# Performance work log

Hardware: AMD Instinct MI355X
Metric: run time of the kernel (lower is better)

## Reference

```python
import jax, jax.numpy as jnp
import numpy as np

B = 262144   # n_batch
DT = 0.01    # filter period T_filter from reset_state


def _quat_mul(q, r):
    # Hamilton product, q,r: [B,4] in (w,x,y,z)
    w1, x1, y1, z1 = q[:, 0], q[:, 1], q[:, 2], q[:, 3]
    w2, x2, y2, z2 = r[:, 0], r[:, 1], r[:, 2], r[:, 3]
    return jnp.stack([
        w1 * w2 - x1 * x2 - y1 * y2 - z1 * z2,
        w1 * x2 + x1 * w2 + y1 * z2 - z1 * y2,
        w1 * y2 - x1 * z2 + y1 * w2 + z1 * x2,
        w1 * z2 + x1 * y2 - y1 * x2 + z1 * w2,
    ], axis=-1)


def _inject(state, err):
    # state: [B,7,1] = [p(3); q(4)], err: [B,6,1] = [dp(3); dtheta(3)]
    p = state[:, :3, 0] + err[:, :3, 0]
    q = state[:, 3:, 0]
    dth = 0.5 * err[:, 3:, 0]
    dq = jnp.concatenate([jnp.ones_like(dth[:, :1]), dth], axis=-1)  # small-angle quat
    qn = _quat_mul(q, dq)
    qn = qn / jnp.linalg.norm(qn, axis=-1, keepdims=True)
    return jnp.concatenate([p, qn], axis=-1)[:, :, None]


def _Xdx(state):
    # ESKF Jacobian of nominal state wrt error state: [B,7,6]
    q = state[:, 3:, 0]
    bsz = q.shape[0]
    w, xq, y, z = q[:, 0], q[:, 1], q[:, 2], q[:, 3]
    Qd = 0.5 * jnp.stack([
        jnp.stack([-xq, -y, -z], -1),
        jnp.stack([w, -z, y], -1),
        jnp.stack([z, w, -xq], -1),
        jnp.stack([-y, xq, w], -1),
    ], axis=1)  # [B,4,3]
    I3 = jnp.broadcast_to(jnp.eye(3, dtype=state.dtype), (bsz, 3, 3))
    top = jnp.concatenate([I3, jnp.zeros((bsz, 3, 3), state.dtype)], axis=-1)
    bot = jnp.concatenate([jnp.zeros((bsz, 4, 3), state.dtype), Qd], axis=-1)
    return jnp.concatenate([top, bot], axis=1)


def setup_inputs() -> dict:
    key = jax.random.key(0)
    k1, k2, k3 = jax.random.split(key, 3)
    x = jax.random.normal(k1, (14, B), dtype=jnp.float32)
    p = jax.random.normal(k2, (B, 3), dtype=jnp.float32)
    q = jax.random.normal(k3, (B, 4), dtype=jnp.float32)
    q = q / jnp.linalg.norm(q, axis=-1, keepdims=True)
    state = jnp.concatenate([p, q], axis=-1)[:, :, None]  # [B,7,1]
    # covariances as in reset_state (diagonal, batched)
    covariance = jnp.tile(jnp.diag(jnp.array([1e-3] * 3 + [0.2] * 3, jnp.float32))[None], (B, 1, 1))
    Q = jnp.tile(jnp.diag(jnp.array([1e-4] * 3 + [2e-4] * 3, jnp.float32))[None], (B, 1, 1))
    R = jnp.tile(jnp.diag(jnp.array([1e-6] * 3 + [1e-4] * 4, jnp.float32))[None], (B, 1, 1))
    return {"x": x, "state": state, "covariance": covariance, "Q": Q, "R": R}


def reference(x, state, covariance, Q, R):
    # --- unpack forward args (mirrors forward(): permute(2,1,0)) ---
    twist = x[8:14].T[:, :, None]        # [B,6,1] control
    measurement = x[0:7].T[:, :, None]   # [B,7,1]
    # --- predict: F = I6, B_matrix = dt * I6 ---
    error_state_prior = DT * twist                       # B_matrix @ u
    predict_state = _inject(state, error_state_prior)    # [B,7,1]
    P = covariance + Q                                   # F P F^T + Q with F = I
    # --- update ---
    H = _Xdx(state)                                      # Hx = I7, so H = Xdx: [B,7,6]
    Ht = jnp.swapaxes(H, 1, 2)                           # [B,6,7]
    S = H @ P @ Ht + R                                   # [B,7,7]
    K = P @ Ht @ jnp.linalg.inv(S)                       # [B,6,7]
    innovation = measurement - predict_state             # [B,7,1]
    error_state = K @ innovation                         # [B,6,1]
    I6 = jnp.eye(6, dtype=P.dtype)
    P_new = (I6[None] - K @ H) @ P                       # stored as self.covariance (side effect)
    new_state = _inject(predict_state, error_state)      # [B,7,1]
    del P_new  # forward() returns only the state
    return new_state
```

## Files before the change

### kernel.cpp

```cpp
#include <hip/hip_runtime.h>

#define DT_C 0.01f

__global__ __launch_bounds__(256) void eskf_kernel(
    const float* __restrict__ x,
    const float* __restrict__ state,
    const float* __restrict__ cov,
    const float* __restrict__ Qm,
    const float* __restrict__ Rm,
    float* __restrict__ out,
    int B)
{
    int b = blockIdx.x * blockDim.x + threadIdx.x;
    if (b >= B) return;

    float meas[7];
#pragma unroll
    for (int i = 0; i < 7; ++i) meas[i] = x[i * B + b];
    float tw[6];
#pragma unroll
    for (int i = 0; i < 6; ++i) tw[i] = x[(8 + i) * B + b];
    float st[7];
#pragma unroll
    for (int i = 0; i < 7; ++i) st[i] = state[b * 7 + i];

    float P[36];
    {
        const float4* c4 = (const float4*)(cov + (size_t)b * 36);
        const float4* q4 = (const float4*)(Qm  + (size_t)b * 36);
#pragma unroll
        for (int i = 0; i < 9; ++i) {
            float4 a = c4[i], bb = q4[i];
            P[4*i+0] = a.x + bb.x;
            P[4*i+1] = a.y + bb.y;
            P[4*i+2] = a.z + bb.z;
            P[4*i+3] = a.w + bb.w;
        }
    }

    float S[7][7];
    {
        const float* r = Rm + (size_t)b * 49;
#pragma unroll
        for (int i = 0; i < 7; ++i)
#pragma unroll
            for (int j = 0; j < 7; ++j)
                S[i][j] = r[i * 7 + j];
    }

    float ps[7];
    {
        float d0 = 0.5f * DT_C * tw[3], d1 = 0.5f * DT_C * tw[4], d2 = 0.5f * DT_C * tw[5];
        ps[0] = st[0] + DT_C * tw[0];
        ps[1] = st[1] + DT_C * tw[1];
        ps[2] = st[2] + DT_C * tw[2];
        float w = st[3], xx = st[4], yy = st[5], zz = st[6];
        float qw = w - xx * d0 - yy * d1 - zz * d2;
        float qx = w * d0 + xx + yy * d2 - zz * d1;
        float qy = w * d1 - xx * d2 + yy + zz * d0;
        float qz = w * d2 + xx * d1 - yy * d0 + zz;
        float inv = rsqrtf(qw * qw + qx * qx + qy * qy + qz * qz);
        ps[3] = qw * inv; ps[4] = qx * inv; ps[5] = qy * inv; ps[6] = qz * inv;
    }

    float Qd[4][3];
    {
        float w = st[3], xx = st[4], yy = st[5], zz = st[6];
        Qd[0][0] = -0.5f * xx; Qd[0][1] = -0.5f * yy; Qd[0][2] = -0.5f * zz;
        Qd[1][0] =  0.5f * w;  Qd[1][1] = -0.5f * zz; Qd[1][2] =  0.5f * yy;
        Qd[2][0] =  0.5f * zz; Qd[2][1] =  0.5f * w;  Qd[2][2] = -0.5f * xx;
        Qd[3][0] = -0.5f * yy; Qd[3][1] =  0.5f * xx; Qd[3][2] =  0.5f * w;
    }

#pragma unroll
    for (int i = 0; i < 3; ++i)
#pragma unroll
        for (int j = 0; j < 3; ++j)
            S[i][j] += P[i * 6 + j];

    float T[4][6];
#pragma unroll
    for (int i = 0; i < 4; ++i)
#pragma unroll
        for (int c = 0; c < 6; ++c) {
            float acc = 0.f;
#pragma unroll
            for (int k = 0; k < 3; ++k) acc += Qd[i][k] * P[(3 + k) * 6 + c];
            T[i][c] = acc;
        }

#pragma unroll
    for (int i = 0; i < 4; ++i)
#pragma unroll
        for (int j = 0; j < 3; ++j) S[3 + i][j] += T[i][j];

#pragma unroll
    for (int i = 0; i < 3; ++i)
#pragma unroll
        for (int j = 0; j < 4; ++j) {
            float acc = 0.f;
#pragma unroll
            for (int k = 0; k < 3; ++k) acc += P[i * 6 + 3 + k] * Qd[j][k];
            S[i][3 + j] += acc;
        }

#pragma unroll
    for (int i = 0; i < 4; ++i)
#pragma unroll
        for (int j = 0; j < 4; ++j) {
            float acc = 0.f;
#pragma unroll
            for (int l = 0; l < 3; ++l) acc += T[i][3 + l] * Qd[j][l];
            S[3 + i][3 + j] += acc;
        }

    float y[7];
#pragma unroll
    for (int i = 0; i < 7; ++i) y[i] = meas[i] - ps[i];

#pragma unroll
    for (int k = 0; k < 7; ++k) {
        float inv = 1.0f / S[k][k];
#pragma unroll
        for (int i = k + 1; i < 7; ++i) {
            float f = S[i][k] * inv;
#pragma unroll
            for (int j = k + 1; j < 7; ++j) S[i][j] -= f * S[k][j];
            y[i] -= f * y[k];
        }
    }
#pragma unroll
    for (int k = 6; k >= 0; --k) {
        float acc = y[k];
#pragma unroll
        for (int j = k + 1; j < 7; ++j) acc -= S[k][j] * y[j];
        y[k] = acc / S[k][k];
    }

    float z6[6];
    z6[0] = y[0]; z6[1] = y[1]; z6[2] = y[2];
#pragma unroll
    for (int c = 0; c < 3; ++c) {
        float acc = 0.f;
#pragma unroll
        for (int i = 0; i < 4; ++i) acc += Qd[i][c] * y[3 + i];
        z6[3 + c] = acc;
    }
    float es[6];
#pragma unroll
    for (int i = 0; i < 6; ++i) {
        float acc = 0.f;
#pragma unroll
        for (int j = 0; j < 6; ++j) acc += P[i * 6 + j] * z6[j];
        es[i] = acc;
    }

    float o0 = ps[0] + es[0];
    float o1 = ps[1] + es[1];
    float o2 = ps[2] + es[2];
    float d0 = 0.5f * es[3], d1 = 0.5f * es[4], d2 = 0.5f * es[5];
    float w = ps[3], xx = ps[4], yy = ps[5], zz = ps[6];
    float qw = w - xx * d0 - yy * d1 - zz * d2;
    float qx = w * d0 + xx + yy * d2 - zz * d1;
    float qy = w * d1 - xx * d2 + yy + zz * d0;
    float qz = w * d2 + xx * d1 - yy * d0 + zz;
    float inv = rsqrtf(qw * qw + qx * qx + qy * qy + qz * qz);

    float* o = out + (size_t)b * 7;
    o[0] = o0; o[1] = o1; o[2] = o2;
    o[3] = qw * inv; o[4] = qx * inv; o[5] = qy * inv; o[6] = qz * inv;
}

extern "C" void kernel_launch(void* const* d_in, const int* in_sizes, int n_in,
                              void* d_out, int out_size, void* d_ws, size_t ws_size,
                              hipStream_t stream) {
    const float* x     = (const float*)d_in[0];
    const float* state = (const float*)d_in[1];
    const float* cov   = (const float*)d_in[2];
    const float* Qm    = (const float*)d_in[3];
    const float* Rm    = (const float*)d_in[4];
    float* out = (float*)d_out;
    int B = in_sizes[1] / 7;
    int block = 256;
    int grid = (B + block - 1) / block;
    eskf_kernel<<<grid, block, 0, stream>>>(x, state, cov, Qm, Rm, out, B);
}
```

Before: 180.7 us.

## Stage state and R loads and output stores through LDS for coalescing

The per-thread strided loads of state (7 floats) and R (49 floats) become coalesced 16-byte global-to-LDS direct loads issued per wave, then each lane reads its row back from LDS. The output is written to LDS and stored as coalesced float4s. Cov and Q loads are issued before the wait so they overlap with the LDS fills, and launch bounds now request 2 blocks per CU. The kernel drops the bounds check and assumes B is a multiple of 256. It also uses about 57 KB of LDS per block, which limits occupancy, and LDS reads at a stride of 49 floats may hit bank conflicts.

```diff
diff --git a/kernel.cpp b/kernel.cpp
--- a/kernel.cpp
+++ b/kernel.cpp
@@ -2,7 +2,14 @@
 
 #define DT_C 0.01f
 
-__global__ __launch_bounds__(256) void eskf_kernel(
+__device__ __forceinline__ void gload_lds16(const float* g, float* l) {
+    __builtin_amdgcn_global_load_lds(
+        (const __attribute__((address_space(1))) void*)g,
+        (__attribute__((address_space(3))) void*)l,
+        16, 0, 0);
+}
+
+__global__ __launch_bounds__(256, 2) void eskf_kernel(
     const float* __restrict__ x,
     const float* __restrict__ state,
     const float* __restrict__ cov,
@@ -11,41 +18,71 @@
     float* __restrict__ out,
     int B)
 {
-    int b = blockIdx.x * blockDim.x + threadIdx.x;
-    if (b >= B) return;
-
-    float meas[7];
-#pragma unroll
-    for (int i = 0; i < 7; ++i) meas[i] = x[i * B + b];
-    float tw[6];
-#pragma unroll
-    for (int i = 0; i < 6; ++i) tw[i] = x[(8 + i) * B + b];
-    float st[7];
-#pragma unroll
-    for (int i = 0; i < 7; ++i) st[i] = state[b * 7 + i];
-
-    float P[36];
+    __shared__ float ldsR[256 * 49];
+    __shared__ float ldsS[256 * 7];
+
+    const int tid  = threadIdx.x;
+    const int lane = tid & 63;
+    const int wave = tid >> 6;
+    const int b    = blockIdx.x * 256 + tid;
+    const int eb   = blockIdx.x * 256 + wave * 64;
+
+    {
+        const float* gs = state + (size_t)eb * 7;
+        float*       ls = ldsS + wave * (64 * 7);
+        gload_lds16(gs + 4 * lane, ls + 4 * lane);
+        if (lane < 48) gload_lds16(gs + 4 * (64 + lane), ls + 4 * (64 + lane));
+
+        const float* gr = Rm + (size_t)eb * 49;
+        float*       lr = ldsR + wave * (64 * 49);
+#pragma unroll
+        for (int k = 0; k < 12; ++k)
+            gload_lds16(gr + 4 * (k * 64 + lane), lr + 4 * (k * 64 + lane));
+        if (lane < 16)
+            gload_lds16(gr + 4 * (768 + lane), lr + 4 * (768 + lane));
+    }
+
+    float4 cv[9], qv[9];
     {
         const float4* c4 = (const float4*)(cov + (size_t)b * 36);
         const float4* q4 = (const float4*)(Qm  + (size_t)b * 36);
 #pragma unroll
-        for (int i = 0; i < 9; ++i) {
-            float4 a = c4[i], bb = q4[i];
-            P[4*i+0] = a.x + bb.x;
-            P[4*i+1] = a.y + bb.y;
-            P[4*i+2] = a.z + bb.z;
-            P[4*i+3] = a.w + bb.w;
-        }
+        for (int i = 0; i < 9; ++i) cv[i] = c4[i];
+#pragma unroll
+        for (int i = 0; i < 9; ++i) qv[i] = q4[i];
+    }
+
+    float meas[7], tw[6];
+#pragma unroll
+    for (int i = 0; i < 7; ++i) meas[i] = x[i * B + b];
+#pragma unroll
+    for (int i = 0; i < 6; ++i) tw[i] = x[(8 + i) * B + b];
+
+    float P[36];
+#pragma unroll
+    for (int i = 0; i < 9; ++i) {
+        P[4 * i + 0] = cv[i].x + qv[i].x;
+        P[4 * i + 1] = cv[i].y + qv[i].y;
+        P[4 * i + 2] = cv[i].z + qv[i].z;
+        P[4 * i + 3] = cv[i].w + qv[i].w;
+    }
+
+    asm volatile("s_waitcnt vmcnt(0)" ::: "memory");
+
+    float st[7];
+    {
+        const float* ls = ldsS + wave * (64 * 7) + lane * 7;
+#pragma unroll
+        for (int i = 0; i < 7; ++i) st[i] = ls[i];
     }
 
     float S[7][7];
     {
-        const float* r = Rm + (size_t)b * 49;
+        const float* lr = ldsR + wave * (64 * 49) + lane * 49;
 #pragma unroll
         for (int i = 0; i < 7; ++i)
 #pragma unroll
-            for (int j = 0; j < 7; ++j)
-                S[i][j] = r[i * 7 + j];
+            for (int j = 0; j < 7; ++j) S[i][j] = lr[i * 7 + j];
     }
 
     float ps[7];
@@ -166,9 +203,17 @@
     float qz = w * d2 + xx * d1 - yy * d0 + zz;
     float inv = rsqrtf(qw * qw + qx * qx + qy * qy + qz * qz);
 
-    float* o = out + (size_t)b * 7;
-    o[0] = o0; o[1] = o1; o[2] = o2;
-    o[3] = qw * inv; o[4] = qx * inv; o[5] = qy * inv; o[6] = qz * inv;
+    {
+        float* ol = ldsS + wave * (64 * 7) + lane * 7;
+        ol[0] = o0; ol[1] = o1; ol[2] = o2;
+        ol[3] = qw * inv; ol[4] = qx * inv; ol[5] = qy * inv; ol[6] = qz * inv;
+        asm volatile("s_waitcnt lgkmcnt(0)" ::: "memory");
+
+        float4*       og = (float4*)(out + (size_t)eb * 7);
+        const float4* lf = (const float4*)(ldsS + wave * (64 * 7));
+        og[lane] = lf[lane];
+        if (lane < 48) og[64 + lane] = lf[64 + lane];
+    }
 }
 
 extern "C" void kernel_launch(void* const* d_in, const int* in_sizes, int n_in,
@@ -181,7 +226,6 @@
     const float* Rm    = (const float*)d_in[4];
     float* out = (float*)d_out;
     int B = in_sizes[1] / 7;
-    int block = 256;
-    int grid = (B + block - 1) / block;
-    eskf_kernel<<<grid, block, 0, stream>>>(x, state, cov, Qm, Rm, out, B);
+    int grid = B / 256;
+    eskf_kernel<<<grid, 256, 0, stream>>>(x, state, cov, Qm, Rm, out, B);
 }
```

Result: faster. 168.6 us (-6.7%).
